# Kernel tuning notes

Hardware: AMD Instinct MI355X
Metric: run time of the kernel (lower is better)

## Reference

```python
import jax, jax.numpy as jnp
import numpy as np

EPS = 1e-5

def _conv3x3(x, w):
    # x: [n,c,h,w], w: [o,c,3,3], stride 1, padding 1 (SAME)
    return jax.lax.conv_general_dilated(x, w, (1, 1), 'SAME',
                                        dimension_numbers=('NCHW', 'OIHW', 'NCHW'))

def _bn(x, g, b, m, v):
    # inference-mode BatchNorm2d with running stats
    s = g / jnp.sqrt(v + EPS)
    return x * s[:, None, None] + (b - m * s)[:, None, None]

def _lrelu(x):
    return jnp.where(x > 0, x, 0.2 * x)

def _conv1x1(x, w, b):
    # w: [o,c] (1x1 conv kernel collapsed)
    return jnp.einsum('nchw,oc->nohw', x, w) + b[:, None, None]

def _conv_relu(x, w, g, b, m, v):
    return _lrelu(_bn(_conv3x3(x, w), g, b, m, v))

def _pam(f, Wq, bq, Wk, bk, Wv, bv, alpha):
    n, c, h, w = f.shape
    hw = h * w
    q = _conv1x1(f, Wq, bq).reshape(n, -1, hw)   # [n,cr,hw]
    k = _conv1x1(f, Wk, bk).reshape(n, -1, hw)   # [n,cr,hw]
    # attention[i,j] over spatial tokens, softmax along j
    attn = jax.nn.softmax(jnp.einsum('nci,ncj->nij', q, k), axis=-1)  # [n,hw,hw]
    v = _conv1x1(f, Wv, bv).reshape(n, c, hw)    # [n,c,hw]
    # torch: bmm(v, attn^T) -> out[:, :, i] = sum_j v[:, :, j] * attn[i, j]
    out = jnp.einsum('ncj,nij->nci', v, attn).reshape(n, c, h, w)
    return alpha * out + f

def _cam(f, W1, b1, W2, b2):
    s = jnp.mean(f, axis=(2, 3), keepdims=True)  # AdaptiveAvgPool2d(1)
    s = _lrelu(_conv1x1(s, W1, b1))
    s = jax.nn.sigmoid(_conv1x1(s, W2, b2))
    return f * s

def _upx2(x):
    n, c, h, w = x.shape
    return jax.image.resize(x, (n, c, 2 * h, 2 * w), 'bilinear')

def setup_inputs() -> dict:
    key = jax.random.key(0)
    ks = jax.random.split(key, 16)
    N, C, H, W_ = 4, 512, 64, 64
    CR, NC = C // 8, 64
    f32 = jnp.float32
    def nrm(k, shape, s=0.05):
        return jax.random.normal(k, shape, f32) * s
    return {
        'x': jax.random.normal(ks[0], (N, C, H, W_), f32),
        'W_pam_in': nrm(ks[1], (C, C, 3, 3)),
        'pam_gamma': jnp.ones((C,), f32), 'pam_beta': jnp.zeros((C,), f32),
        'pam_mean': nrm(ks[2], (C,)), 'pam_var': jax.random.uniform(ks[3], (C,), f32) + 0.5,
        'Wq': nrm(ks[4], (CR, C)), 'bq': jnp.zeros((CR,), f32),
        'Wk': nrm(ks[5], (CR, C)), 'bk': jnp.zeros((CR,), f32),
        'Wv': nrm(ks[6], (C, C)), 'bv': jnp.zeros((C,), f32),
        'alpha': nrm(ks[7], (1,), 1.0),
        'W_pam_out': nrm(ks[8], (NC, C)), 'b_pam_out': jnp.zeros((NC,), f32),
        'W_cam_in': nrm(ks[9], (C, C, 3, 3)),
        'cam_gamma': jnp.ones((C,), f32), 'cam_beta': jnp.zeros((C,), f32),
        'cam_mean': nrm(ks[10], (C,)), 'cam_var': jax.random.uniform(ks[11], (C,), f32) + 0.5,
        'Wc1': nrm(ks[12], (CR, C)), 'bc1': jnp.zeros((CR,), f32),
        'Wc2': nrm(ks[13], (C, CR)), 'bc2': jnp.zeros((C,), f32),
        'W_cam_out': nrm(ks[14], (NC, C)), 'b_cam_out': jnp.zeros((NC,), f32),
    }

def reference(x, W_pam_in, pam_gamma, pam_beta, pam_mean, pam_var,
              Wq, bq, Wk, bk, Wv, bv, alpha, W_pam_out, b_pam_out,
              W_cam_in, cam_gamma, cam_beta, cam_mean, cam_var,
              Wc1, bc1, Wc2, bc2, W_cam_out, b_cam_out):
    pam_feat = _conv_relu(x, W_pam_in, pam_gamma, pam_beta, pam_mean, pam_var)
    pam_feat = _pam(pam_feat, Wq, bq, Wk, bk, Wv, bv, alpha)
    pam_feat = _upx2(_conv1x1(pam_feat, W_pam_out, b_pam_out))
    cam_feat = _conv_relu(x, W_cam_in, cam_gamma, cam_beta, cam_mean, cam_var)
    cam_feat = _cam(cam_feat, Wc1, bc1, Wc2, bc2)
    cam_feat = _upx2(_conv1x1(cam_feat, W_cam_out, b_cam_out))
    return pam_feat + cam_feat
```

## Files before the change

### kernel.cpp

```cpp
#include <hip/hip_runtime.h>
#include <hip/hip_bf16.h>
#include <math.h>

#define N_  4
#define C_  512
#define H_  64
#define W_  64
#define HW_ 4096
#define CR_ 64
#define NC_ 64
#define EPSV 1e-5f

typedef __attribute__((ext_vector_type(8))) __bf16 bf16x8;
typedef __attribute__((ext_vector_type(4))) float f32x4;
typedef __hip_bfloat16 bf16s;

__device__ __forceinline__ unsigned short bfb(float f) {
    union { bf16s h; unsigned short u; } cv;
    cv.h = __float2bfloat16(f);
    return cv.u;
}

__device__ __forceinline__ float b2f(unsigned short h) {
    union { unsigned u; float f; } c; c.u = ((unsigned)h) << 16; return c.f;
}

__device__ __forceinline__ int swz8(int row, int ch) {
    return row * 64 + ((ch ^ (row & 7)) << 3);
}

__global__ __launch_bounds__(256) void k_xpose(
    const float* __restrict__ x, bf16s* __restrict__ xbT)
{
    __shared__ float xs[64][65];
    const int tid = threadIdx.x;
    const int n = blockIdx.z, c0 = blockIdx.y * 64, p0 = blockIdx.x * 64;
    for (int e = tid; e < 4096; e += 256) {
        int ci = e >> 6, pi = e & 63;
        xs[ci][pi] = x[((size_t)(n*C_ + c0 + ci))*HW_ + p0 + pi];
    }
    __syncthreads();
    for (int e = tid; e < 4096; e += 256) {
        int pi = e >> 6, ci = e & 63;
        xbT[((size_t)n*HW_ + p0 + pi)*C_ + c0 + ci] = __float2bfloat16(xs[ci][pi]);
    }
}

__global__ __launch_bounds__(256) void k_wprep(
    const float* __restrict__ w, bf16s* __restrict__ wb)
{
    int e = blockIdx.x * 256 + threadIdx.x;
    int c = e & 511; int r = e >> 9;
    int tap = r % 9; int o = r / 9;
    wb[e] = __float2bfloat16(w[((size_t)o*C_ + c)*9 + tap]);
}

__global__ __launch_bounds__(256) void k_wcast(
    const float* __restrict__ in, bf16s* __restrict__ out, int nElem)
{
    int e = blockIdx.x * 256 + threadIdx.x;
    if (e < nElem) out[e] = __float2bfloat16(in[e]);
}

__global__ __launch_bounds__(256, 3) void k_conv3x3_mfma(
    const bf16s* __restrict__ xbT,
    const bf16s* __restrict__ wb,  const bf16s* __restrict__ wb2,
    const float* __restrict__ gamma,  const float* __restrict__ beta,
    const float* __restrict__ mean,   const float* __restrict__ var,
    const float* __restrict__ gamma2, const float* __restrict__ beta2,
    const float* __restrict__ mean2,  const float* __restrict__ var2,
    bf16s* __restrict__ featT, bf16s* __restrict__ featT2,
    float* __restrict__ csum)
{
    __shared__ bf16s aL[3][128][36];
    __shared__ bf16s bL[132][36];
    const int tid = threadIdx.x;
    const int lid = blockIdx.x + (blockIdx.y << 5) + (blockIdx.z << 8);
    const int xcd = lid & 7;
    const int half = xcd >> 2;
    const int n    = xcd & 3;
    const int w8   = lid >> 3;
    const int o0 = (w8 >> 5) * 128;
    const int pt = w8 & 31;
    const int y0 = pt * 2;
    const bf16s* wbs = half ? wb2 : wb;
    const float* gm = half ? gamma2 : gamma;
    const float* bt = half ? beta2  : beta;
    const float* mn = half ? mean2  : mean;
    const float* vr = half ? var2   : var;
    bf16s* ft = half ? featT2 : featT;
    const int lane = tid & 63;
    const int wid  = tid >> 6;
    const int wr = wid >> 1, wc = wid & 1;
    const int lr = lane & 15, cb = lane >> 4;

    const int ao  = tid >> 2;
    const int ac  = (tid & 3) * 8;
    const int t0  = tid >> 2;
    const int t1  = t0 + 64;
    const int t2  = t0 + 128;
    const int ry1 = t1 >= 66 ? 1 : 0;
    const int xi1 = t1 - (ry1 ? 66 : 0);

    f32x4 acc[4][4];
#pragma unroll
    for (int i = 0; i < 4; ++i)
#pragma unroll
        for (int j = 0; j < 4; ++j) acc[i][j] = (f32x4){0.f,0.f,0.f,0.f};

    int4 pA0, pA1, pA2, pA3, pA4, pA5, pB0, pB1, pB2;

#define CONV_AADDR(DXI, OHALF, C0, DYI) \
    (const int4*)(wbs + ((size_t)(o0 + (OHALF) + ao)*9 + (DYI)*3 + (DXI))*C_ + (C0) + ac)

#define CONV_BLOAD(DST, RY, XI, C0, DYI, VALID)                               \
    {                                                                         \
        int row_ = y0 + (DYI) - 1 + (RY);                                     \
        int xc_  = (XI) - 1;                                                  \
        int4 v_ = {0,0,0,0};                                                  \
        if ((VALID) && row_ >= 0 && row_ < H_ && xc_ >= 0 && xc_ < W_)        \
            v_ = *(const int4*)(xbT +                                         \
                ((size_t)n*HW_ + row_*W_ + xc_)*C_ + (C0) + ac);              \
        DST = v_;                                                             \
    }

#define CONV_ISSUE(C0, DYI)                                                   \
    {                                                                         \
        pA0 = *CONV_AADDR(0,  0, C0, DYI);                                    \
        pA1 = *CONV_AADDR(0, 64, C0, DYI);                                    \
        pA2 = *CONV_AADDR(1,  0, C0, DYI);                                    \
        pA3 = *CONV_AADDR(1, 64, C0, DYI);                                    \
        pA4 = *CONV_AADDR(2,  0, C0, DYI);                                    \
        pA5 = *CONV_AADDR(2, 64, C0, DYI);                                    \
        CONV_BLOAD(pB0, 0, t0, C0, DYI, 1)                                    \
        CONV_BLOAD(pB1, ry1, xi1, C0, DYI, 1)                                 \
        CONV_BLOAD(pB2, 1, t2 - 66, C0, DYI, tid < 16)                        \
    }

    CONV_ISSUE(0, 0)
    int c0 = 0, dyi = 0;
    for (int it = 0; it < 48; ++it) {
        *(int4*)&aL[0][ao][ac]      = pA0;
        *(int4*)&aL[0][64 + ao][ac] = pA1;
        *(int4*)&aL[1][ao][ac]      = pA2;
        *(int4*)&aL[1][64 + ao][ac] = pA3;
        *(int4*)&aL[2][ao][ac]      = pA4;
        *(int4*)&aL[2][64 + ao][ac] = pA5;
        *(int4*)&bL[t0][ac] = pB0;
        *(int4*)&bL[t1][ac] = pB1;
        if (tid < 16) *(int4*)&bL[t2][ac] = pB2;
        __syncthreads();
        int nd = dyi + 1, nc = c0;
        if (nd == 3) { nd = 0; nc += 32; }
        if (it < 47) CONV_ISSUE(nc, nd)
#pragma unroll
        for (int dxi = 0; dxi < 3; ++dxi) {
            bf16x8 af[4], bfv[4];
#pragma unroll
            for (int fm = 0; fm < 4; ++fm)
                af[fm] = *(const bf16x8*)&aL[dxi][wr*64 + fm*16 + lr][cb*8];
#pragma unroll
            for (int fn = 0; fn < 4; ++fn) {
                int pg = wc*64 + fn*16 + lr;
                int ry = pg >> 6, xc = pg & 63;
                bfv[fn] = *(const bf16x8*)&bL[ry*66 + xc + dxi][cb*8];
            }
#pragma unroll
            for (int fm = 0; fm < 4; ++fm)
#pragma unroll
                for (int fn = 0; fn < 4; ++fn)
                    acc[fm][fn] = __builtin_amdgcn_mfma_f32_16x16x32_bf16(
                        af[fm], bfv[fn], acc[fm][fn], 0, 0, 0);
        }
        __syncthreads();
        c0 = nc; dyi = nd;
    }
#undef CONV_ISSUE
#undef CONV_BLOAD
#undef CONV_AADDR
#pragma unroll
    for (int fm = 0; fm < 4; ++fm) {
        float sc[4], sh[4];
        const int obase = o0 + wr*64 + fm*16 + cb*4;
#pragma unroll
        for (int r = 0; r < 4; ++r) {
            int o = obase + r;
            sc[r] = gm[o] * rsqrtf(vr[o] + EPSV);
            sh[r] = bt[o] - mn[o]*sc[r];
        }
        float ps[4] = {0.f, 0.f, 0.f, 0.f};
#pragma unroll
        for (int fn = 0; fn < 4; ++fn) {
            int pg = wc*64 + fn*16 + lr;
            int p  = pt*128 + pg;
            float vv[4];
#pragma unroll
            for (int r = 0; r < 4; ++r) {
                float t = fmaf(acc[fm][fn][r], sc[r], sh[r]);
                vv[r] = t > 0.f ? t : 0.2f*t;
                ps[r] += vv[r];
            }
            uint2 u;
            u.x = (unsigned)bfb(vv[0]) | ((unsigned)bfb(vv[1]) << 16);
            u.y = (unsigned)bfb(vv[2]) | ((unsigned)bfb(vv[3]) << 16);
            *(uint2*)&ft[((size_t)n*HW_ + p)*C_ + obase] = u;
        }
        if (half) {
#pragma unroll
            for (int r = 0; r < 4; ++r) {
                float s = ps[r];
                s += __shfl_xor(s, 1);
                s += __shfl_xor(s, 2);
                s += __shfl_xor(s, 4);
                s += __shfl_xor(s, 8);
                if (lr == 0) atomicAdd(&csum[n*C_ + obase + r], s);
            }
        }
    }
}

__global__ __launch_bounds__(256, 2) void k_gemm_qkv(
    const bf16s* __restrict__ Wqk, const bf16s* __restrict__ Wv,
    const bf16s* __restrict__ Bt,
    const float* __restrict__ bq, const float* __restrict__ bk,
    const float* __restrict__ bv,
    bf16s* __restrict__ qkb, bf16s* __restrict__ vb)
{
    __shared__ bf16s aL[64][36];
    __shared__ bf16s bL[256][36];
    const int tid = threadIdx.x;
    const int flat = blockIdx.x + (blockIdx.y << 4) + blockIdx.z * 160;
    const int k8 = flat & 7;
    const int n  = k8 >> 1;
    const int xh = k8 & 1;
    const int w8 = flat >> 3;
    const int yy = w8 % 10;
    const int p0 = ((((w8 / 10) << 1) | xh)) << 8;
    const bool isqk = (yy < 2);
    const int o0 = isqk ? yy*64 : (yy - 2)*64;
    const bf16s* A = isqk ? Wqk : Wv;
    const int lane = tid & 63;
    const int wid  = tid >> 6;
    const int lr = lane & 15, cb = lane >> 4;
    const int arow = tid >> 2, ach = (tid & 3) * 8;

    f32x4 acc[4][4];
#pragma unroll
    for (int i = 0; i < 4; ++i)
#pragma unroll
        for (int j = 0; j < 4; ++j) acc[i][j] = (f32x4){0.f,0.f,0.f,0.f};

    int4 pA, pB0, pB1, pB2, pB3;

#define GEMM_ISSUE(C0)                                                        \
    {                                                                         \
        pA = *(const int4*)&A[(size_t)(o0 + arow)*C_ + (C0) + ach];           \
        pB0 = *(const int4*)&Bt[((size_t)n*HW_ + p0 + arow      )*C_ + (C0) + ach]; \
        pB1 = *(const int4*)&Bt[((size_t)n*HW_ + p0 + arow +  64)*C_ + (C0) + ach]; \
        pB2 = *(const int4*)&Bt[((size_t)n*HW_ + p0 + arow + 128)*C_ + (C0) + ach]; \
        pB3 = *(const int4*)&Bt[((size_t)n*HW_ + p0 + arow + 192)*C_ + (C0) + ach]; \
    }

    GEMM_ISSUE(0)
    for (int c0 = 0; c0 < C_; c0 += 32) {
        *(int4*)&aL[arow][ach] = pA;
        *(int4*)&bL[arow      ][ach] = pB0;
        *(int4*)&bL[arow +  64][ach] = pB1;
        *(int4*)&bL[arow + 128][ach] = pB2;
        *(int4*)&bL[arow + 192][ach] = pB3;
        __syncthreads();
        if (c0 + 32 < C_) GEMM_ISSUE(c0 + 32)
        bf16x8 af[4], bfv[4];
#pragma unroll
        for (int fo = 0; fo < 4; ++fo)
            af[fo] = *(const bf16x8*)&aL[fo*16 + lr][cb*8];
#pragma unroll
        for (int fp = 0; fp < 4; ++fp)
            bfv[fp] = *(const bf16x8*)&bL[wid*64 + fp*16 + lr][cb*8];
#pragma unroll
        for (int fo = 0; fo < 4; ++fo)
#pragma unroll
            for (int fp = 0; fp < 4; ++fp)
                acc[fo][fp] = __builtin_amdgcn_mfma_f32_16x16x32_bf16(
                    af[fo], bfv[fp], acc[fo][fp], 0, 0, 0);
        __syncthreads();
    }
#undef GEMM_ISSUE
#pragma unroll
    for (int fo = 0; fo < 4; ++fo) {
        const int obase = o0 + fo*16 + cb*4;
        const float* bp = isqk ? ((obase >> 6) ? bk : bq) : bv;
        const int bofs = isqk ? (obase & 63) : obase;
        float bv4[4];
#pragma unroll
        for (int r = 0; r < 4; ++r) bv4[r] = bp[bofs + r];
#pragma unroll
        for (int fp = 0; fp < 4; ++fp) {
            int p = p0 + wid*64 + fp*16 + lr;
            float v[4];
#pragma unroll
            for (int r = 0; r < 4; ++r) v[r] = acc[fo][fp][r] + bv4[r];
            if (isqk) {
                uint2 u;
                u.x = (unsigned)bfb(v[0]) | ((unsigned)bfb(v[1]) << 16);
                u.y = (unsigned)bfb(v[2]) | ((unsigned)bfb(v[3]) << 16);
                size_t base = (((size_t)((obase >> 6) * N_ + n))*HW_ + p)*64
                              + (obase & 63);
                *(uint2*)&qkb[base] = u;
            } else {
#pragma unroll
                for (int r = 0; r < 4; ++r)
                    vb[((size_t)(n*C_ + obase + r))*HW_ + p] =
                        __float2bfloat16(v[r]);
            }
        }
    }
}

__global__ __launch_bounds__(256, 2) void k_gemm_tail(
    const bf16s* __restrict__ Wpob, const bf16s* __restrict__ Wcob,
    const bf16s* __restrict__ featT, const bf16s* __restrict__ featT2,
    const float* __restrict__ b_pam, const float* __restrict__ b_cam,
    const float* __restrict__ s2,
    float* __restrict__ pam_low, float* __restrict__ cam_low)
{
    __shared__ bf16s aL[64][36];
    __shared__ bf16s bL[256][36];
    const int tid = threadIdx.x;
    const int half = blockIdx.y;
    const int n  = blockIdx.z;
    const int p0 = blockIdx.x * 256;
    const bf16s* A = half ? Wcob : Wpob;
    const bf16s* Bt = half ? featT2 : featT;
    const float* bias = half ? b_cam : b_pam;
    const float* scale = half ? s2 : nullptr;
    float* outp = half ? cam_low : pam_low;
    const int lane = tid & 63;
    const int wid  = tid >> 6;
    const int lr = lane & 15, cb = lane >> 4;
    const int arow = tid >> 2, ach = (tid & 3) * 8;

    f32x4 acc[4][4];
#pragma unroll
    for (int i = 0; i < 4; ++i)
#pragma unroll
        for (int j = 0; j < 4; ++j) acc[i][j] = (f32x4){0.f,0.f,0.f,0.f};

    int4 pA, pB0, pB1, pB2, pB3;
    float4 pS0, pS1;

#define GEMM_ISSUE(C0)                                                        \
    {                                                                         \
        pA = *(const int4*)&A[(size_t)arow*C_ + (C0) + ach];                  \
        if (scale) {                                                          \
            pS0 = *(const float4*)&scale[(size_t)n*C_ + (C0) + ach];          \
            pS1 = *(const float4*)&scale[(size_t)n*C_ + (C0) + ach + 4];      \
        }                                                                     \
        pB0 = *(const int4*)&Bt[((size_t)n*HW_ + p0 + arow      )*C_ + (C0) + ach]; \
        pB1 = *(const int4*)&Bt[((size_t)n*HW_ + p0 + arow +  64)*C_ + (C0) + ach]; \
        pB2 = *(const int4*)&Bt[((size_t)n*HW_ + p0 + arow + 128)*C_ + (C0) + ach]; \
        pB3 = *(const int4*)&Bt[((size_t)n*HW_ + p0 + arow + 192)*C_ + (C0) + ach]; \
    }

    GEMM_ISSUE(0)
    for (int c0 = 0; c0 < C_; c0 += 32) {
        if (scale) {
            const bf16s* sp = (const bf16s*)&pA;
            bf16s tmp[8];
            tmp[0] = __float2bfloat16(__bfloat162float(sp[0]) * pS0.x);
            tmp[1] = __float2bfloat16(__bfloat162float(sp[1]) * pS0.y);
            tmp[2] = __float2bfloat16(__bfloat162float(sp[2]) * pS0.z);
            tmp[3] = __float2bfloat16(__bfloat162float(sp[3]) * pS0.w);
            tmp[4] = __float2bfloat16(__bfloat162float(sp[4]) * pS1.x);
            tmp[5] = __float2bfloat16(__bfloat162float(sp[5]) * pS1.y);
            tmp[6] = __float2bfloat16(__bfloat162float(sp[6]) * pS1.z);
            tmp[7] = __float2bfloat16(__bfloat162float(sp[7]) * pS1.w);
            *(int4*)&aL[arow][ach] = *(int4*)tmp;
        } else {
            *(int4*)&aL[arow][ach] = pA;
        }
        *(int4*)&bL[arow      ][ach] = pB0;
        *(int4*)&bL[arow +  64][ach] = pB1;
        *(int4*)&bL[arow + 128][ach] = pB2;
        *(int4*)&bL[arow + 192][ach] = pB3;
        __syncthreads();
        if (c0 + 32 < C_) GEMM_ISSUE(c0 + 32)
        bf16x8 af[4], bfv[4];
#pragma unroll
        for (int fo = 0; fo < 4; ++fo)
            af[fo] = *(const bf16x8*)&aL[fo*16 + lr][cb*8];
#pragma unroll
        for (int fp = 0; fp < 4; ++fp)
            bfv[fp] = *(const bf16x8*)&bL[wid*64 + fp*16 + lr][cb*8];
#pragma unroll
        for (int fo = 0; fo < 4; ++fo)
#pragma unroll
            for (int fp = 0; fp < 4; ++fp)
                acc[fo][fp] = __builtin_amdgcn_mfma_f32_16x16x32_bf16(
                    af[fo], bfv[fp], acc[fo][fp], 0, 0, 0);
        __syncthreads();
    }
#undef GEMM_ISSUE
#pragma unroll
    for (int fo = 0; fo < 4; ++fo) {
        const int obase = fo*16 + cb*4;
        float bv[4];
#pragma unroll
        for (int r = 0; r < 4; ++r) bv[r] = bias[obase + r];
#pragma unroll
        for (int fp = 0; fp < 4; ++fp) {
            int p = p0 + wid*64 + fp*16 + lr;
#pragma unroll
            for (int r = 0; r < 4; ++r)
                outp[((size_t)(n*NC_ + obase + r))*HW_ + p] =
                    acc[fo][fp][r] + bv[r];
        }
    }
}

__global__ __launch_bounds__(256) void k_rowstats_mfma(
    const bf16s* __restrict__ qb, const bf16s* __restrict__ kb,
    float* __restrict__ rowm, float* __restrict__ rowl)
{
    __shared__ bf16s qs[4096];
    __shared__ bf16s ks[2][4096];
    const int tid = threadIdx.x;
    const int lid = blockIdx.x + (blockIdx.y << 6) + (blockIdx.z << 8);
    const int n  = lid & 3;
    const int jz = (lid >> 2) & 1;
    const int i0 = (lid >> 3) << 6;
    const int lane = tid & 63;
    const int wid  = tid >> 6;
    const int lr = lane & 15, cb = lane >> 4;

    for (int e = tid; e < 512; e += 256) {
        int row = e >> 3, ch = e & 7;
        *(int4*)&qs[swz8(row, ch)] =
            *(const int4*)&qb[((size_t)n*HW_ + i0 + row)*CR_ + ch*8];
    }
    const int krow = tid >> 3, kch = tid & 7;
    const bf16s* kbase = kb + (size_t)n*HW_*CR_ + (size_t)jz*2048*CR_ + kch*8;
    int4 kreg0 = *(const int4*)(kbase + (size_t)krow*CR_);
    int4 kreg1 = *(const int4*)(kbase + (size_t)(krow + 32)*CR_);
    *(int4*)&ks[0][swz8(krow, kch)] = kreg0;
    *(int4*)&ks[0][swz8(krow + 32, kch)] = kreg1;
    kreg0 = *(const int4*)(kbase + (size_t)(64 + krow)*CR_);
    kreg1 = *(const int4*)(kbase + (size_t)(64 + krow + 32)*CR_);
    __syncthreads();
    bf16x8 bq[2];
#pragma unroll
    for (int kk = 0; kk < 2; ++kk)
        bq[kk] = *(const bf16x8*)&qs[swz8(wid*16 + lr, kk*4 + cb)];

    float m_t = -INFINITY, l_t = 0.f;
    for (int t = 0; t < 32; ++t) {
        const bf16s* kst = ks[t & 1];
        f32x4 sv[4];
#pragma unroll
        for (int fj = 0; fj < 4; ++fj) {
            f32x4 s = (f32x4){0.f,0.f,0.f,0.f};
#pragma unroll
            for (int kk = 0; kk < 2; ++kk) {
                bf16x8 ak = *(const bf16x8*)&kst[swz8(fj*16 + lr, kk*4 + cb)];
                s = __builtin_amdgcn_mfma_f32_16x16x32_bf16(ak, bq[kk], s, 0, 0, 0);
            }
            sv[fj] = s;
        }
        if (t < 31) {
            *(int4*)&ks[(t + 1) & 1][swz8(krow, kch)] = kreg0;
            *(int4*)&ks[(t + 1) & 1][swz8(krow + 32, kch)] = kreg1;
            if (t < 30) {
                kreg0 = *(const int4*)(kbase + (size_t)((t+2)*64 + krow)*CR_);
                kreg1 = *(const int4*)(kbase + (size_t)((t+2)*64 + krow + 32)*CR_);
            }
        }
        float mx = m_t;
#pragma unroll
        for (int fj = 0; fj < 4; ++fj)
#pragma unroll
            for (int r = 0; r < 4; ++r) mx = fmaxf(mx, sv[fj][r]);
        float sum = 0.f;
#pragma unroll
        for (int fj = 0; fj < 4; ++fj)
#pragma unroll
            for (int r = 0; r < 4; ++r) sum += __expf(sv[fj][r] - mx);
        l_t = l_t * __expf(m_t - mx) + sum;
        m_t = mx;
        __syncthreads();
    }
#pragma unroll
    for (int mask = 16; mask <= 32; mask <<= 1) {
        float mo = __shfl_xor(m_t, mask);
        float lo = __shfl_xor(l_t, mask);
        float m2 = fmaxf(m_t, mo);
        l_t = l_t * __expf(m_t - m2) + lo * __expf(mo - m2);
        m_t = m2;
    }
    if (cb == 0) {
        rowm[((size_t)jz*N_ + n)*HW_ + i0 + wid*16 + lr] = m_t;
        rowl[((size_t)jz*N_ + n)*HW_ + i0 + wid*16 + lr] = l_t;
    }
}

__global__ __launch_bounds__(256, 4) void k_pv_mfma(
    const bf16s* __restrict__ qb, const bf16s* __restrict__ kb,
    const bf16s* __restrict__ vb, const float* __restrict__ rowm,
    const float* __restrict__ rowl, const float* __restrict__ alpha,
    bf16s* __restrict__ featT)
{
    __shared__ bf16s ks[2][4096];
    __shared__ bf16s ps[2][4096];
    const int tid = threadIdx.x;
    const int lid = blockIdx.x + (blockIdx.y << 6) + (blockIdx.z << 8);
    const int k8  = lid & 7;
    const int n   = k8 >> 1;
    const int cc0 = (((lid >> 3) & 1) * 2 + (k8 & 1)) << 7;
    const int i0  = (lid >> 4) << 6;
    const int lane = tid & 63;
    const int wid  = tid >> 6;
    const int lr = lane & 15, cb = lane >> 4;

    for (int e = tid; e < 512; e += 256) {
        int row = e >> 3, ch = e & 7;
        *(int4*)&ks[0][swz8(row, ch)] =
            *(const int4*)&qb[((size_t)n*HW_ + i0 + row)*CR_ + ch*8];
    }
    const int krow = tid >> 3, kch = tid & 7;
    const bf16s* kbase = kb + (size_t)n*HW_*CR_ + kch*8;
    int4 kreg0 = *(const int4*)(kbase + (size_t)krow*CR_);
    int4 kreg1 = *(const int4*)(kbase + (size_t)(krow + 32)*CR_);
    __syncthreads();
    bf16x8 bq[2];
#pragma unroll
    for (int kk = 0; kk < 2; ++kk)
        bq[kk] = *(const bf16x8*)&ks[0][swz8(wid*16 + lr, kk*4 + cb)];

    const size_t sidx = (size_t)n*HW_ + i0 + wid*16 + lr;
    const float m0 = rowm[sidx], m1 = rowm[sidx + (size_t)N_*HW_];
    const float l0 = rowl[sidx], l1 = rowl[sidx + (size_t)N_*HW_];
    const float mreg = fmaxf(m0, m1);
    const float rinv = 1.f / (l0*__expf(m0 - mreg) + l1*__expf(m1 - mreg));
    const float al = alpha[0];
    __syncthreads();
    *(int4*)&ks[0][swz8(krow, kch)] = kreg0;
    *(int4*)&ks[0][swz8(krow + 32, kch)] = kreg1;
    kreg0 = *(const int4*)(kbase + (size_t)(64 + krow)*CR_);
    kreg1 = *(const int4*)(kbase + (size_t)(64 + krow + 32)*CR_);
    __syncthreads();

    f32x4 acc[2][4];
#pragma unroll
    for (int i = 0; i < 2; ++i)
#pragma unroll
        for (int j = 0; j < 4; ++j) acc[i][j] = (f32x4){0.f,0.f,0.f,0.f};

    const bf16s* vbase = vb + ((size_t)(n*C_ + cc0 + wid*32))*HW_;
    bf16x8 vc0, vc1, vc2, vc3, vn0, vn1, vn2, vn3;

    for (int jt = 0; jt < 64; ++jt) {
        const bf16s* vj = vbase + jt*64;
        vn0 = *(const bf16x8*)(vj + (size_t)(     lr)*HW_      + cb*8);
        vn1 = *(const bf16x8*)(vj + (size_t)(16 + lr)*HW_      + cb*8);
        vn2 = *(const bf16x8*)(vj + (size_t)(     lr)*HW_ + 32 + cb*8);
        vn3 = *(const bf16x8*)(vj + (size_t)(16 + lr)*HW_ + 32 + cb*8);
        if (jt > 0) {
            const bf16s* pp = ps[(jt - 1) & 1];
            bf16x8 pa[4];
#pragma unroll
            for (int fi = 0; fi < 4; ++fi)
                pa[fi] = *(const bf16x8*)&pp[swz8(fi*16 + lr, cb)];
#pragma unroll
            for (int fi = 0; fi < 4; ++fi) {
                acc[0][fi] = __builtin_amdgcn_mfma_f32_16x16x32_bf16(
                    vc0, pa[fi], acc[0][fi], 0, 0, 0);
                acc[1][fi] = __builtin_amdgcn_mfma_f32_16x16x32_bf16(
                    vc1, pa[fi], acc[1][fi], 0, 0, 0);
            }
#pragma unroll
            for (int fi = 0; fi < 4; ++fi)
                pa[fi] = *(const bf16x8*)&pp[swz8(fi*16 + lr, 4 + cb)];
#pragma unroll
            for (int fi = 0; fi < 4; ++fi) {
                acc[0][fi] = __builtin_amdgcn_mfma_f32_16x16x32_bf16(
                    vc2, pa[fi], acc[0][fi], 0, 0, 0);
                acc[1][fi] = __builtin_amdgcn_mfma_f32_16x16x32_bf16(
                    vc3, pa[fi], acc[1][fi], 0, 0, 0);
            }
        }
        {
            const bf16s* kst = ks[jt & 1];
            bf16s* pst = ps[jt & 1];
#pragma unroll
            for (int fj = 0; fj < 4; ++fj) {
                f32x4 s = (f32x4){0.f,0.f,0.f,0.f};
#pragma unroll
                for (int kk = 0; kk < 2; ++kk) {
                    bf16x8 ak = *(const bf16x8*)&kst[swz8(fj*16 + lr, kk*4 + cb)];
                    s = __builtin_amdgcn_mfma_f32_16x16x32_bf16(ak, bq[kk], s, 0, 0, 0);
                }
                unsigned short b[4];
#pragma unroll
                for (int r = 0; r < 4; ++r)
                    b[r] = bfb(__expf(s[r] - mreg) * rinv);
                uint2 u;
                u.x = (unsigned)b[0] | ((unsigned)b[1] << 16);
                u.y = (unsigned)b[2] | ((unsigned)b[3] << 16);
                *(uint2*)&pst[swz8(wid*16 + lr, fj*2 + (cb >> 1)) + (cb & 1)*4] = u;
            }
        }
        if (jt < 63) {
            *(int4*)&ks[(jt + 1) & 1][swz8(krow, kch)] = kreg0;
            *(int4*)&ks[(jt + 1) & 1][swz8(krow + 32, kch)] = kreg1;
            if (jt < 62) {
                kreg0 = *(const int4*)(kbase + (size_t)((jt+2)*64 + krow)*CR_);
                kreg1 = *(const int4*)(kbase + (size_t)((jt+2)*64 + krow + 32)*CR_);
            }
        }
        vc0 = vn0; vc1 = vn1; vc2 = vn2; vc3 = vn3;
        __syncthreads();
    }
    {
        const bf16s* pp = ps[63 & 1];
        bf16x8 pa[4];
#pragma unroll
        for (int fi = 0; fi < 4; ++fi)
            pa[fi] = *(const bf16x8*)&pp[swz8(fi*16 + lr, cb)];
#pragma unroll
        for (int fi = 0; fi < 4; ++fi) {
            acc[0][fi] = __builtin_amdgcn_mfma_f32_16x16x32_bf16(
                vc0, pa[fi], acc[0][fi], 0, 0, 0);
            acc[1][fi] = __builtin_amdgcn_mfma_f32_16x16x32_bf16(
                vc1, pa[fi], acc[1][fi], 0, 0, 0);
        }
#pragma unroll
        for (int fi = 0; fi < 4; ++fi)
            pa[fi] = *(const bf16x8*)&pp[swz8(fi*16 + lr, 4 + cb)];
#pragma unroll
        for (int fi = 0; fi < 4; ++fi) {
            acc[0][fi] = __builtin_amdgcn_mfma_f32_16x16x32_bf16(
                vc2, pa[fi], acc[0][fi], 0, 0, 0);
            acc[1][fi] = __builtin_amdgcn_mfma_f32_16x16x32_bf16(
                vc3, pa[fi], acc[1][fi], 0, 0, 0);
        }
    }
#pragma unroll
    for (int fc2 = 0; fc2 < 2; ++fc2) {
        const int ccl = wid*32 + fc2*16 + cb*4;
#pragma unroll
        for (int fi = 0; fi < 4; ++fi) {
            const int p = i0 + fi*16 + lr;
            bf16s* fb = &featT[((size_t)n*HW_ + p)*C_ + cc0 + ccl];
            uint2 fv = *(const uint2*)fb;
            float f0 = b2f((unsigned short)(fv.x & 0xffff));
            float f1 = b2f((unsigned short)(fv.x >> 16));
            float f2 = b2f((unsigned short)(fv.y & 0xffff));
            float f3 = b2f((unsigned short)(fv.y >> 16));
            float v0 = fmaf(al, acc[fc2][fi][0], f0);
            float v1 = fmaf(al, acc[fc2][fi][1], f1);
            float v2 = fmaf(al, acc[fc2][fi][2], f2);
            float v3 = fmaf(al, acc[fc2][fi][3], f3);
            uint2 u;
            u.x = (unsigned)bfb(v0) | ((unsigned)bfb(v1) << 16);
            u.y = (unsigned)bfb(v2) | ((unsigned)bfb(v3) << 16);
            *(uint2*)fb = u;
        }
    }
}

__global__ __launch_bounds__(64) void k_cmlp(
    const float* __restrict__ s0, const float* __restrict__ Wc1,
    const float* __restrict__ bc1, const float* __restrict__ Wc2,
    const float* __restrict__ bc2, float* __restrict__ s2)
{
    const int n = blockIdx.x, tid = threadIdx.x;
    __shared__ float s1s[64];
    float a = 0.f;
    for (int c = 0; c < C_; ++c)
        a = fmaf(Wc1[(size_t)tid*C_ + c], s0[n*C_ + c] * (1.f/HW_), a);
    a += bc1[tid];
    a = a > 0.f ? a : 0.2f*a;
    s1s[tid] = a;
    __syncthreads();
    for (int c = tid; c < C_; c += 64) {
        float b = 0.f;
        for (int i = 0; i < CR_; ++i) b = fmaf(Wc2[(size_t)c*CR_ + i], s1s[i], b);
        b += bc2[c];
        s2[n*C_ + c] = 1.f / (1.f + __expf(-b));
    }
}

__global__ __launch_bounds__(256) void k_up(
    const float* __restrict__ pl, const float* __restrict__ cl,
    float* __restrict__ out)
{
    int idx = blockIdx.x * 256 + threadIdx.x;
    int ox = idx & 127; int rest = idx >> 7;
    int oy = rest & 127; rest >>= 7;
    int o  = rest & 63;  int n = rest >> 6;
    float fy = oy*0.5f - 0.25f;
    float fx = ox*0.5f - 0.25f;
    int y0 = (int)floorf(fy); float wy = fy - y0;
    int x0 = (int)floorf(fx); float wx = fx - x0;
    int y0c = y0 < 0 ? 0 : y0;      int y1c = y0+1 > 63 ? 63 : y0+1;
    int x0c = x0 < 0 ? 0 : x0;      int x1c = x0+1 > 63 ? 63 : x0+1;
    const float* a = pl + ((size_t)(n*NC_ + o))*HW_;
    const float* b = cl + ((size_t)(n*NC_ + o))*HW_;
    float v00 = a[y0c*64+x0c] + b[y0c*64+x0c];
    float v01 = a[y0c*64+x1c] + b[y0c*64+x1c];
    float v10 = a[y1c*64+x0c] + b[y1c*64+x0c];
    float v11 = a[y1c*64+x1c] + b[y1c*64+x1c];
    out[idx] = (1.f-wy)*((1.f-wx)*v00 + wx*v01) + wy*((1.f-wx)*v10 + wx*v11);
}

extern "C" void kernel_launch(void* const* d_in, const int* in_sizes, int n_in,
                              void* d_out, int out_size, void* d_ws, size_t ws_size,
                              hipStream_t stream)
{
    const float* x         = (const float*)d_in[0];
    const float* W_pam_in  = (const float*)d_in[1];
    const float* pam_g     = (const float*)d_in[2];
    const float* pam_b     = (const float*)d_in[3];
    const float* pam_m     = (const float*)d_in[4];
    const float* pam_v     = (const float*)d_in[5];
    const float* Wq        = (const float*)d_in[6];
    const float* bq        = (const float*)d_in[7];
    const float* Wk        = (const float*)d_in[8];
    const float* bk        = (const float*)d_in[9];
    const float* Wv        = (const float*)d_in[10];
    const float* bv        = (const float*)d_in[11];
    const float* alpha     = (const float*)d_in[12];
    const float* W_pam_out = (const float*)d_in[13];
    const float* b_pam_out = (const float*)d_in[14];
    const float* W_cam_in  = (const float*)d_in[15];
    const float* cam_g     = (const float*)d_in[16];
    const float* cam_b     = (const float*)d_in[17];
    const float* cam_m     = (const float*)d_in[18];
    const float* cam_v     = (const float*)d_in[19];
    const float* Wc1       = (const float*)d_in[20];
    const float* bc1       = (const float*)d_in[21];
    const float* Wc2       = (const float*)d_in[22];
    const float* bc2       = (const float*)d_in[23];
    const float* W_cam_out = (const float*)d_in[24];
    const float* b_cam_out = (const float*)d_in[25];

    float* pam_low = (float*)d_ws;
    float* rowm    = pam_low + 1048576;
    float* rowl    = rowm    + 32768;
    float* s0      = rowl    + 32768;
    float* s2      = s0      + 2048;
    bf16s* xbT     = (bf16s*)(s2 + 2048);
    bf16s* featTb  = xbT + 8388608;
    bf16s* featTb2 = featTb + 8388608;
    bf16s* vb      = featTb2 + 8388608;
    bf16s* qb      = vb + 8388608;
    bf16s* kb      = qb + 1048576;
    bf16s* wbp     = kb + 1048576;
    bf16s* wbp2    = wbp + 2359296;
    bf16s* Wqb     = wbp2 + 2359296;
    bf16s* Wkb     = Wqb + 32768;
    bf16s* Wvb     = Wkb + 32768;
    bf16s* Wpob    = Wvb + 262144;
    bf16s* Wcob    = Wpob + 32768;
    float* cam_low = (float*)qb;

    dim3 b256(256);
    k_xpose<<<dim3(64,8,4), b256, 0, stream>>>(x, xbT);
    k_wcast<<<dim3(128), b256, 0, stream>>>(Wq, Wqb, 32768);
    k_wcast<<<dim3(128), b256, 0, stream>>>(Wk, Wkb, 32768);
    k_wcast<<<dim3(1024), b256, 0, stream>>>(Wv, Wvb, 262144);
    k_wcast<<<dim3(128), b256, 0, stream>>>(W_pam_out, Wpob, 32768);
    k_wcast<<<dim3(128), b256, 0, stream>>>(W_cam_out, Wcob, 32768);
    hipMemsetAsync(s0, 0, 2048*sizeof(float), stream);
    k_wprep<<<dim3(9216), b256, 0, stream>>>(W_pam_in, wbp);
    k_wprep<<<dim3(9216), b256, 0, stream>>>(W_cam_in, wbp2);
    k_conv3x3_mfma<<<dim3(32,8,4), b256, 0, stream>>>(
        xbT, wbp, wbp2, pam_g, pam_b, pam_m, pam_v,
        cam_g, cam_b, cam_m, cam_v, featTb, featTb2, s0);
    k_gemm_qkv<<<dim3(16,10,4), b256, 0, stream>>>(
        Wqb, Wvb, featTb, bq, bk, bv, qb, vb);
    k_rowstats_mfma<<<dim3(64,4,2), b256, 0, stream>>>(qb, kb, rowm, rowl);
    k_cmlp<<<dim3(4), dim3(64), 0, stream>>>(s0, Wc1, bc1, Wc2, bc2, s2);
    k_pv_mfma<<<dim3(64,4,4), b256, 0, stream>>>(
        qb, kb, vb, rowm, rowl, alpha, featTb);
    k_gemm_tail<<<dim3(16,2,4), b256, 0, stream>>>(
        Wpob, Wcob, featTb, featTb2, b_pam_out, b_cam_out, s2,
        pam_low, cam_low);
    k_up<<<dim3(16384), b256, 0, stream>>>(pam_low, cam_low, (float*)d_out);
}
```

Measured before the change: 441.4 us.

## Fuse softmax row statistics into PV kernel via online softmax rescaling

Removes the separate row-statistics kernel that computed per-row max and sum over all keys, and instead keeps a running max and sum inside the PV kernel, flash-attention style. The accumulators are rescaled each tile by a factor passed through shared memory, and the output is divided by the final sum. This drops a full extra QK^T pass and its launch, at the cost of per-tile cross-lane reductions, extra exponentials and accumulator rescaling in the main loop. The rowstats pass was also computed only once per row, while PV blocks recompute QK^T per channel group, so the added in-loop work is spread across every channel-split block.

Result: no change. 433.1 us (-1.9%).

```diff
diff --git a/kernel.cpp b/kernel.cpp
--- a/kernel.cpp
+++ b/kernel.cpp
@@ -418,98 +418,15 @@
     }
 }
 
-__global__ __launch_bounds__(256) void k_rowstats_mfma(
-    const bf16s* __restrict__ qb, const bf16s* __restrict__ kb,
-    float* __restrict__ rowm, float* __restrict__ rowl)
-{
-    __shared__ bf16s qs[4096];
-    __shared__ bf16s ks[2][4096];
-    const int tid = threadIdx.x;
-    const int lid = blockIdx.x + (blockIdx.y << 6) + (blockIdx.z << 8);
-    const int n  = lid & 3;
-    const int jz = (lid >> 2) & 1;
-    const int i0 = (lid >> 3) << 6;
-    const int lane = tid & 63;
-    const int wid  = tid >> 6;
-    const int lr = lane & 15, cb = lane >> 4;
-
-    for (int e = tid; e < 512; e += 256) {
-        int row = e >> 3, ch = e & 7;
-        *(int4*)&qs[swz8(row, ch)] =
-            *(const int4*)&qb[((size_t)n*HW_ + i0 + row)*CR_ + ch*8];
-    }
-    const int krow = tid >> 3, kch = tid & 7;
-    const bf16s* kbase = kb + (size_t)n*HW_*CR_ + (size_t)jz*2048*CR_ + kch*8;
-    int4 kreg0 = *(const int4*)(kbase + (size_t)krow*CR_);
-    int4 kreg1 = *(const int4*)(kbase + (size_t)(krow + 32)*CR_);
-    *(int4*)&ks[0][swz8(krow, kch)] = kreg0;
-    *(int4*)&ks[0][swz8(krow + 32, kch)] = kreg1;
-    kreg0 = *(const int4*)(kbase + (size_t)(64 + krow)*CR_);
-    kreg1 = *(const int4*)(kbase + (size_t)(64 + krow + 32)*CR_);
-    __syncthreads();
-    bf16x8 bq[2];
-#pragma unroll
-    for (int kk = 0; kk < 2; ++kk)
-        bq[kk] = *(const bf16x8*)&qs[swz8(wid*16 + lr, kk*4 + cb)];
-
-    float m_t = -INFINITY, l_t = 0.f;
-    for (int t = 0; t < 32; ++t) {
-        const bf16s* kst = ks[t & 1];
-        f32x4 sv[4];
-#pragma unroll
-        for (int fj = 0; fj < 4; ++fj) {
-            f32x4 s = (f32x4){0.f,0.f,0.f,0.f};
-#pragma unroll
-            for (int kk = 0; kk < 2; ++kk) {
-                bf16x8 ak = *(const bf16x8*)&kst[swz8(fj*16 + lr, kk*4 + cb)];
-                s = __builtin_amdgcn_mfma_f32_16x16x32_bf16(ak, bq[kk], s, 0, 0, 0);
-            }
-            sv[fj] = s;
-        }
-        if (t < 31) {
-            *(int4*)&ks[(t + 1) & 1][swz8(krow, kch)] = kreg0;
-            *(int4*)&ks[(t + 1) & 1][swz8(krow + 32, kch)] = kreg1;
-            if (t < 30) {
-                kreg0 = *(const int4*)(kbase + (size_t)((t+2)*64 + krow)*CR_);
-                kreg1 = *(const int4*)(kbase + (size_t)((t+2)*64 + krow + 32)*CR_);
-            }
-        }
-        float mx = m_t;
-#pragma unroll
-        for (int fj = 0; fj < 4; ++fj)
-#pragma unroll
-            for (int r = 0; r < 4; ++r) mx = fmaxf(mx, sv[fj][r]);
-        float sum = 0.f;
-#pragma unroll
-        for (int fj = 0; fj < 4; ++fj)
-#pragma unroll
-            for (int r = 0; r < 4; ++r) sum += __expf(sv[fj][r] - mx);
-        l_t = l_t * __expf(m_t - mx) + sum;
-        m_t = mx;
-        __syncthreads();
-    }
-#pragma unroll
-    for (int mask = 16; mask <= 32; mask <<= 1) {
-        float mo = __shfl_xor(m_t, mask);
-        float lo = __shfl_xor(l_t, mask);
-        float m2 = fmaxf(m_t, mo);
-        l_t = l_t * __expf(m_t - m2) + lo * __expf(mo - m2);
-        m_t = m2;
-    }
-    if (cb == 0) {
-        rowm[((size_t)jz*N_ + n)*HW_ + i0 + wid*16 + lr] = m_t;
-        rowl[((size_t)jz*N_ + n)*HW_ + i0 + wid*16 + lr] = l_t;
-    }
-}
-
 __global__ __launch_bounds__(256, 4) void k_pv_mfma(
     const bf16s* __restrict__ qb, const bf16s* __restrict__ kb,
-    const bf16s* __restrict__ vb, const float* __restrict__ rowm,
-    const float* __restrict__ rowl, const float* __restrict__ alpha,
+    const bf16s* __restrict__ vb, const float* __restrict__ alpha,
     bf16s* __restrict__ featT)
 {
     __shared__ bf16s ks[2][4096];
     __shared__ bf16s ps[2][4096];
+    __shared__ float sfl[2][64];
+    __shared__ float lfin[64];
     const int tid = threadIdx.x;
     const int lid = blockIdx.x + (blockIdx.y << 6) + (blockIdx.z << 8);
     const int k8  = lid & 7;
@@ -535,11 +452,6 @@
     for (int kk = 0; kk < 2; ++kk)
         bq[kk] = *(const bf16x8*)&ks[0][swz8(wid*16 + lr, kk*4 + cb)];
 
-    const size_t sidx = (size_t)n*HW_ + i0 + wid*16 + lr;
-    const float m0 = rowm[sidx], m1 = rowm[sidx + (size_t)N_*HW_];
-    const float l0 = rowl[sidx], l1 = rowl[sidx + (size_t)N_*HW_];
-    const float mreg = fmaxf(m0, m1);
-    const float rinv = 1.f / (l0*__expf(m0 - mreg) + l1*__expf(m1 - mreg));
     const float al = alpha[0];
     __syncthreads();
     *(int4*)&ks[0][swz8(krow, kch)] = kreg0;
@@ -554,6 +466,8 @@
 #pragma unroll
         for (int j = 0; j < 4; ++j) acc[i][j] = (f32x4){0.f,0.f,0.f,0.f};
 
+    float m_run = -INFINITY, l_run = 0.f;
+
     const bf16s* vbase = vb + ((size_t)(n*C_ + cc0 + wid*32))*HW_;
     bf16x8 vc0, vc1, vc2, vc3, vn0, vn1, vn2, vn3;
 
@@ -564,8 +478,18 @@
         vn2 = *(const bf16x8*)(vj + (size_t)(     lr)*HW_ + 32 + cb*8);
         vn3 = *(const bf16x8*)(vj + (size_t)(16 + lr)*HW_ + 32 + cb*8);
         if (jt > 0) {
+            const float* fs = sfl[(jt - 1) & 1];
             const bf16s* pp = ps[(jt - 1) & 1];
             bf16x8 pa[4];
+#pragma unroll
+            for (int fi = 0; fi < 4; ++fi) {
+                const float f = fs[fi*16 + lr];
+#pragma unroll
+                for (int r = 0; r < 4; ++r) {
+                    acc[0][fi][r] *= f;
+                    acc[1][fi][r] *= f;
+                }
+            }
 #pragma unroll
             for (int fi = 0; fi < 4; ++fi)
                 pa[fi] = *(const bf16x8*)&pp[swz8(fi*16 + lr, cb)];
@@ -590,23 +514,57 @@
         {
             const bf16s* kst = ks[jt & 1];
             bf16s* pst = ps[jt & 1];
-#pragma unroll
-            for (int fj = 0; fj < 4; ++fj) {
-                f32x4 s = (f32x4){0.f,0.f,0.f,0.f};
-#pragma unroll
-                for (int kk = 0; kk < 2; ++kk) {
-                    bf16x8 ak = *(const bf16x8*)&kst[swz8(fj*16 + lr, kk*4 + cb)];
-                    s = __builtin_amdgcn_mfma_f32_16x16x32_bf16(ak, bq[kk], s, 0, 0, 0);
-                }
-                unsigned short b[4];
-#pragma unroll
-                for (int r = 0; r < 4; ++r)
-                    b[r] = bfb(__expf(s[r] - mreg) * rinv);
-                uint2 u;
-                u.x = (unsigned)b[0] | ((unsigned)b[1] << 16);
-                u.y = (unsigned)b[2] | ((unsigned)b[3] << 16);
-                *(uint2*)&pst[swz8(wid*16 + lr, fj*2 + (cb >> 1)) + (cb & 1)*4] = u;
-            }
+            f32x4 sv0 = (f32x4){0.f,0.f,0.f,0.f};
+            f32x4 sv1 = (f32x4){0.f,0.f,0.f,0.f};
+            f32x4 sv2 = (f32x4){0.f,0.f,0.f,0.f};
+            f32x4 sv3 = (f32x4){0.f,0.f,0.f,0.f};
+            sv0 = __builtin_amdgcn_mfma_f32_16x16x32_bf16(
+                *(const bf16x8*)&kst[swz8(     lr, cb)], bq[0], sv0, 0, 0, 0);
+            sv0 = __builtin_amdgcn_mfma_f32_16x16x32_bf16(
+                *(const bf16x8*)&kst[swz8(     lr, 4 + cb)], bq[1], sv0, 0, 0, 0);
+            sv1 = __builtin_amdgcn_mfma_f32_16x16x32_bf16(
+                *(const bf16x8*)&kst[swz8(16 + lr, cb)], bq[0], sv1, 0, 0, 0);
+            sv1 = __builtin_amdgcn_mfma_f32_16x16x32_bf16(
+                *(const bf16x8*)&kst[swz8(16 + lr, 4 + cb)], bq[1], sv1, 0, 0, 0);
+            sv2 = __builtin_amdgcn_mfma_f32_16x16x32_bf16(
+                *(const bf16x8*)&kst[swz8(32 + lr, cb)], bq[0], sv2, 0, 0, 0);
+            sv2 = __builtin_amdgcn_mfma_f32_16x16x32_bf16(
+                *(const bf16x8*)&kst[swz8(32 + lr, 4 + cb)], bq[1], sv2, 0, 0, 0);
+            sv3 = __builtin_amdgcn_mfma_f32_16x16x32_bf16(
+                *(const bf16x8*)&kst[swz8(48 + lr, cb)], bq[0], sv3, 0, 0, 0);
+            sv3 = __builtin_amdgcn_mfma_f32_16x16x32_bf16(
+                *(const bf16x8*)&kst[swz8(48 + lr, 4 + cb)], bq[1], sv3, 0, 0, 0);
+            float tmax = sv0[0];
+#pragma unroll
+            for (int r = 0; r < 4; ++r) {
+                tmax = fmaxf(tmax, sv0[r]); tmax = fmaxf(tmax, sv1[r]);
+                tmax = fmaxf(tmax, sv2[r]); tmax = fmaxf(tmax, sv3[r]);
+            }
+            tmax = fmaxf(tmax, __shfl_xor(tmax, 16));
+            tmax = fmaxf(tmax, __shfl_xor(tmax, 32));
+            const float mnew = fmaxf(m_run, tmax);
+            const float fsc  = __expf(m_run - mnew);
+            m_run = mnew;
+            float tsum = 0.f;
+#define PV_PACK(SV, FJ)                                                       \
+            {                                                                 \
+                float p0_ = __expf(SV[0] - mnew), p1_ = __expf(SV[1] - mnew); \
+                float p2_ = __expf(SV[2] - mnew), p3_ = __expf(SV[3] - mnew); \
+                tsum += (p0_ + p1_) + (p2_ + p3_);                            \
+                uint2 u;                                                      \
+                u.x = (unsigned)bfb(p0_) | ((unsigned)bfb(p1_) << 16);        \
+                u.y = (unsigned)bfb(p2_) | ((unsigned)bfb(p3_) << 16);        \
+                *(uint2*)&pst[swz8(wid*16 + lr, FJ*2 + (cb >> 1)) + (cb & 1)*4] = u; \
+            }
+            PV_PACK(sv0, 0)
+            PV_PACK(sv1, 1)
+            PV_PACK(sv2, 2)
+            PV_PACK(sv3, 3)
+#undef PV_PACK
+            tsum += __shfl_xor(tsum, 16);
+            tsum += __shfl_xor(tsum, 32);
+            l_run = l_run * fsc + tsum;
+            if (cb == 0) sfl[jt & 1][wid*16 + lr] = fsc;
         }
         if (jt < 63) {
             *(int4*)&ks[(jt + 1) & 1][swz8(krow, kch)] = kreg0;
@@ -619,9 +577,20 @@
         vc0 = vn0; vc1 = vn1; vc2 = vn2; vc3 = vn3;
         __syncthreads();
     }
+    if (cb == 0) lfin[wid*16 + lr] = l_run;
     {
-        const bf16s* pp = ps[63 & 1];
+        const float* fs = sfl[1];
+        const bf16s* pp = ps[1];
         bf16x8 pa[4];
+#pragma unroll
+        for (int fi = 0; fi < 4; ++fi) {
+            const float f = fs[fi*16 + lr];
+#pragma unroll
+            for (int r = 0; r < 4; ++r) {
+                acc[0][fi][r] *= f;
+                acc[1][fi][r] *= f;
+            }
+        }
 #pragma unroll
         for (int fi = 0; fi < 4; ++fi)
             pa[fi] = *(const bf16x8*)&pp[swz8(fi*16 + lr, cb)];
@@ -643,22 +612,24 @@
                 vc3, pa[fi], acc[1][fi], 0, 0, 0);
         }
     }
+    __syncthreads();
 #pragma unroll
     for (int fc2 = 0; fc2 < 2; ++fc2) {
         const int ccl = wid*32 + fc2*16 + cb*4;
 #pragma unroll
         for (int fi = 0; fi < 4; ++fi) {
             const int p = i0 + fi*16 + lr;
+            const float rv = al / lfin[fi*16 + lr];
             bf16s* fb = &featT[((size_t)n*HW_ + p)*C_ + cc0 + ccl];
             uint2 fv = *(const uint2*)fb;
             float f0 = b2f((unsigned short)(fv.x & 0xffff));
             float f1 = b2f((unsigned short)(fv.x >> 16));
             float f2 = b2f((unsigned short)(fv.y & 0xffff));
             float f3 = b2f((unsigned short)(fv.y >> 16));
-            float v0 = fmaf(al, acc[fc2][fi][0], f0);
-            float v1 = fmaf(al, acc[fc2][fi][1], f1);
-            float v2 = fmaf(al, acc[fc2][fi][2], f2);
-            float v3 = fmaf(al, acc[fc2][fi][3], f3);
+            float v0 = fmaf(rv, acc[fc2][fi][0], f0);
+            float v1 = fmaf(rv, acc[fc2][fi][1], f1);
+            float v2 = fmaf(rv, acc[fc2][fi][2], f2);
+            float v3 = fmaf(rv, acc[fc2][fi][3], f3);
             uint2 u;
             u.x = (unsigned)bfb(v0) | ((unsigned)bfb(v1) << 16);
             u.y = (unsigned)bfb(v2) | ((unsigned)bfb(v3) << 16);
@@ -744,9 +715,7 @@
     const float* b_cam_out = (const float*)d_in[25];
 
     float* pam_low = (float*)d_ws;
-    float* rowm    = pam_low + 1048576;
-    float* rowl    = rowm    + 32768;
-    float* s0      = rowl    + 32768;
+    float* s0      = pam_low + 1048576;
     float* s2      = s0      + 2048;
     bf16s* xbT     = (bf16s*)(s2 + 2048);
     bf16s* featTb  = xbT + 8388608;
@@ -778,10 +747,9 @@
         cam_g, cam_b, cam_m, cam_v, featTb, featTb2, s0);
     k_gemm_qkv<<<dim3(16,10,4), b256, 0, stream>>>(
         Wqb, Wvb, featTb, bq, bk, bv, qb, vb);
-    k_rowstats_mfma<<<dim3(64,4,2), b256, 0, stream>>>(qb, kb, rowm, rowl);
     k_cmlp<<<dim3(4), dim3(64), 0, stream>>>(s0, Wc1, bc1, Wc2, bc2, s2);
     k_pv_mfma<<<dim3(64,4,4), b256, 0, stream>>>(
-        qb, kb, vb, rowm, rowl, alpha, featTb);
+        qb, kb, vb, alpha, featTb);
     k_gemm_tail<<<dim3(16,2,4), b256, 0, stream>>>(
         Wpob, Wcob, featTb, featTb2, b_pam_out, b_cam_out, s2,
         pam_low, cam_low);
```
